# Kernel tuning notes

Measured on AMD Instinct MI355X. Metric: run time of the kernel, lower is better.

Reference implementation:

```python
import jax, jax.numpy as jnp
import numpy as np

N = 8192
N_DIM = 7
N_WIDTH = 64


def setup_inputs() -> dict:
    key = jax.random.key(0)
    ks = jax.random.split(key, 12)
    scale = 0.05
    u = lambda k, shape: scale * (2.0 * jax.random.uniform(k, shape) - 1.0)
    # Linear params stored as (in, out) so forward uses x @ W + b (same math as torch Linear).
    lin = lambda k, fan_in, fan_out: (
        jax.random.uniform(jax.random.fold_in(k, 0), (fan_in, fan_out),
                           minval=-1.0, maxval=1.0) / np.sqrt(fan_in),
        jax.random.uniform(jax.random.fold_in(k, 1), (fan_out,),
                           minval=-1.0, maxval=1.0) / np.sqrt(fan_in),
    )
    W1, b1 = lin(ks[1], N_DIM, N_WIDTH)
    W2, b2 = lin(ks[2], N_WIDTH, N_WIDTH)
    Wl, bl = lin(ks[3], N_WIDTH, 1)
    return {
        "x": jax.random.normal(ks[0], (N, N_DIM), dtype=jnp.float32),
        "alpha": jax.random.uniform(ks[4], (1,)),          # Edges.alpha = 1 * rand(1)
        "W1": W1, "b1": b1, "wt1": u(ks[5], (N_WIDTH, N_WIDTH)), "bs1": u(ks[6], (1,)),
        "W2": W2, "b2": b2, "wt2": u(ks[7], (N_WIDTH, N_WIDTH)), "bs2": u(ks[8], (1,)),
        "Wl": Wl, "bl": bl,
    }


def _edges(x, alpha):
    eta, phi = x[:, 1], x[:, 2]
    deta = eta[:, None] - eta[None, :]                      # (n, n)
    dphi = jnp.abs(phi[:, None] - phi[None, :])
    dphi = jnp.where(dphi > jnp.pi, 2.0 * jnp.pi - dphi, dphi)
    dRdR = deta * deta + dphi * dphi
    A = jnp.exp(-alpha[0] * dRdR)
    return jax.nn.softmax(A, axis=1) + jnp.eye(x.shape[0], dtype=x.dtype)


def _gcn_layer(X, A, W, b, wt, bs):
    X = jax.nn.relu(X @ W + b)                              # embed + relu
    X = (A @ X) @ wt + bs[0]                                # aggregate + mix + scalar bias
    return jax.nn.relu(X)


def reference(x, alpha, W1, b1, wt1, bs1, W2, b2, wt2, bs2, Wl, bl):
    A = _edges(x, alpha)
    V = jax.nn.relu(_gcn_layer(x, A, W1, b1, wt1, bs1))
    V = jax.nn.relu(_gcn_layer(V, A, W2, b2, wt2, bs2))
    s = V.sum(axis=0)                                       # (n_width,)
    return jax.nn.sigmoid(s @ Wl + bl)                      # (1,)
```

## Files before the change

kernel.cpp:

```cpp
#include <hip/hip_runtime.h>
#include <math.h>

#define NN 8192
#define L2E 1.44269504088896340736f
#define TWO_PI 6.28318530717958647693f

typedef _Float16 h8 __attribute__((ext_vector_type(8)));
typedef float f32x4 __attribute__((ext_vector_type(4)));
#define MFMA16(A, B, C) __builtin_amdgcn_mfma_f32_16x16x32_f16(A, B, C, 0, 0, 0)

#define GLD_LDS16(gsrc, ldst)                                          \
  __builtin_amdgcn_global_load_lds(                                    \
      (const __attribute__((address_space(1))) unsigned int*)(gsrc),   \
      (__attribute__((address_space(3))) unsigned int*)(ldst), 16, 0, 0)

union V8 { float4 v[2]; float f[8]; };
union AF { h8 v; decltype(__builtin_amdgcn_cvt_pkrtz(0.f, 0.f)) p[4]; };

__global__ __launch_bounds__(256) void prep_kernel(
    const float* __restrict__ x, const float* __restrict__ alpha,
    const float* __restrict__ W1, const float* __restrict__ b1,
    float* __restrict__ eta_s, float* __restrict__ phi_s,
    float* __restrict__ H1, _Float16* __restrict__ HT1,
    float* __restrict__ svec)
{
  __shared__ float sW[448];
  __shared__ float sb[64];
  __shared__ float T[32][65];
  const int t = threadIdx.x;
  if (blockIdx.x == 0 && t < 64) svec[t] = 0.f;
  for (int k = t; k < 448; k += 256) sW[k] = W1[k];
  if (t < 64) sb[t] = b1[t];
  const float s = sqrtf(alpha[0] * L2E);
  const int i0 = blockIdx.x * 32;
  const int r = t >> 3, q = t & 7;
  const int i = i0 + r;
  float xv[7];
#pragma unroll
  for (int k = 0; k < 7; k++) xv[k] = x[i * 7 + k];
  if (q == 0) { eta_s[i] = xv[1] * s; phi_s[i] = xv[2] * s; }
  __syncthreads();
#pragma unroll
  for (int c = 0; c < 8; c++) {
    const int n = q * 8 + c;
    float hv = sb[n];
#pragma unroll
    for (int k = 0; k < 7; k++) hv = fmaf(xv[k], sW[k * 64 + n], hv);
    T[r][n] = fmaxf(hv, 0.f);
  }
  __syncthreads();
  for (int e = t; e < 2048; e += 256) H1[i0 * 64 + e] = T[e >> 6][e & 63];
  const int n = t >> 2, sg = (t & 3) * 8;
  h8 v;
#pragma unroll
  for (int ss = 0; ss < 8; ss++) v[ss] = (_Float16)T[sg + ss][n];
  *(h8*)(HT1 + (size_t)n * NN + i0 + sg) = v;
}

template <int PASS>
__global__ __launch_bounds__(512, 4) void fused_pass(
    const float* __restrict__ eta_s, const float* __restrict__ phi_s,
    const _Float16* __restrict__ HTin, const float* __restrict__ Hres,
    const float* __restrict__ WA, const float* __restrict__ bsA,
    const float* __restrict__ WB, const float* __restrict__ bB,
    const float* __restrict__ alpha, float* __restrict__ lsum,
    float* __restrict__ Hout, _Float16* __restrict__ HTout,
    float* __restrict__ svec, const float* __restrict__ Wl,
    const float* __restrict__ bl, float* __restrict__ out,
    unsigned* __restrict__ bar)
{
  __shared__ __align__(16) char smem[65536];
  __shared__ unsigned last_ticket;
  _Float16* stage = (_Float16*)smem;
  const int tid = threadIdx.x;
  const int w = tid >> 6, lane = tid & 63, m = lane & 15, g = lane >> 4;
  const int i0 = blockIdx.x << 4;
  const float Cs = TWO_PI * sqrtf(alpha[0] * L2E);
  const float et0 = eta_s[i0 + m], ph0 = phi_s[i0 + m];

  const int rr = tid >> 5, gq = tid & 31;
  const _Float16* sb4[4];
#pragma unroll
  for (int k = 0; k < 4; ++k) {
    const int rowk = k * 16 + rr;
    sb4[k] = HTin + (size_t)rowk * NN + ((gq ^ (rowk & 31)) << 3);
  }
  int fo[4];
#pragma unroll
  for (int c = 0; c < 4; ++c) {
    const int row = c * 16 + m;
    fo[c] = row * 256 + ((((w << 2) | g) ^ (row & 31)) << 3);
  }

  f32x4 a0 = {0,0,0,0}, a1 = {0,0,0,0}, a2 = {0,0,0,0}, a3 = {0,0,0,0};
  float lacc = 0.f;

  const float* ep = eta_s + (w << 5) + (g << 3);
  const float* pp = phi_s + (w << 5) + (g << 3);
  V8 E, P, En, Pn;
  E.v[0] = *(const float4*)ep;  E.v[1] = *(const float4*)(ep + 4);
  P.v[0] = *(const float4*)pp;  P.v[1] = *(const float4*)(pp + 4);
  En = E; Pn = P;

#pragma unroll
  for (int k = 0; k < 4; ++k)
    GLD_LDS16(sb4[k], stage + ((k * 512 + tid) << 3));
  __syncthreads();

  for (int s = 0; s < 32; ++s) {
    _Float16* cur = stage + ((s & 1) << 14);
    if (s < 31) {
      _Float16* nxt = stage + (((s + 1) & 1) << 14);
      const int joff = (s + 1) * 256;
#pragma unroll
      for (int k = 0; k < 4; ++k)
        GLD_LDS16(sb4[k] + joff, nxt + ((k * 512 + tid) << 3));
      ep += 256; pp += 256;
      En.v[0] = *(const float4*)ep;  En.v[1] = *(const float4*)(ep + 4);
      Pn.v[0] = *(const float4*)pp;  Pn.v[1] = *(const float4*)(pp + 4);
    }
    const h8 b0 = *(const h8*)(cur + fo[0]);
    const h8 b1 = *(const h8*)(cur + fo[1]);
    const h8 b2 = *(const h8*)(cur + fo[2]);
    const h8 b3 = *(const h8*)(cur + fo[3]);

    AF af;
#pragma unroll
    for (int tt = 0; tt < 8; tt += 2) {
      float Pv[2];
#pragma unroll
      for (int u = 0; u < 2; ++u) {
        const float dp = ph0 - P.f[tt + u];
        const float ad = fabsf(dp);
        const float wr = fminf(ad, Cs - ad);
        const float de = et0 - E.f[tt + u];
        const float r2 = fmaf(de, de, wr * wr);
        const float a  = __builtin_amdgcn_exp2f(-r2);
        const float pv = __builtin_amdgcn_exp2f(fmaf(a, L2E, -L2E));
        if constexpr (PASS == 1) lacc += pv;
        Pv[u] = pv;
      }
      af.p[tt >> 1] = __builtin_amdgcn_cvt_pkrtz(Pv[0], Pv[1]);
    }
    a0 = MFMA16(af.v, b0, a0); a1 = MFMA16(af.v, b1, a1);
    a2 = MFMA16(af.v, b2, a2); a3 = MFMA16(af.v, b3, a3);
    E = En; P = Pn;
    __syncthreads();
  }

  float* RED  = (float*)smem;
  float* LRED = (float*)(smem + 34816);
  float* LROW = (float*)(smem + 36864);
  float* UBUF = (float*)(smem + 37120);
  float* ZBUF = (float*)(smem + 41728);

#pragma unroll
  for (int r = 0; r < 4; ++r) {
    const int rowi = (w * 16 + g * 4 + r) * 68;
    RED[rowi + m]      = a0[r];
    RED[rowi + 16 + m] = a1[r];
    RED[rowi + 32 + m] = a2[r];
    RED[rowi + 48 + m] = a3[r];
  }
  if constexpr (PASS == 1) LRED[((w << 2) | g) * 16 + m] = lacc;
  __syncthreads();

  const int r  = tid >> 5;
  const int c2 = (tid & 31) << 1;
  float y0 = 0.f, y1 = 0.f;
#pragma unroll
  for (int q = 0; q < 8; ++q) {
    y0 += RED[(q * 16 + r) * 68 + c2];
    y1 += RED[(q * 16 + r) * 68 + c2 + 1];
  }
  const float2 hres = *(const float2*)(Hres + (size_t)(i0 + r) * 64 + c2);
  if (tid < 16) {
    float lv;
    if constexpr (PASS == 1) {
      lv = 0.f;
#pragma unroll
      for (int q = 0; q < 32; ++q) lv += LRED[q * 16 + tid];
      lsum[i0 + tid] = lv;
    } else {
      lv = lsum[i0 + tid];
    }
    LROW[tid] = lv;
  }
  __syncthreads();

  const float rl = 1.0f / LROW[r];
  UBUF[r * 68 + c2]     = fmaf(y0, rl, hres.x);
  UBUF[r * 68 + c2 + 1] = fmaf(y1, rl, hres.y);
  __syncthreads();

  float z0 = bsA[0], z1 = z0;
  for (int k = 0; k < 64; ++k) {
    const float uk = UBUF[r * 68 + k];
    const float2 wv = *(const float2*)(WA + k * 64 + c2);
    z0 = fmaf(uk, wv.x, z0);
    z1 = fmaf(uk, wv.y, z1);
  }
  z0 = fmaxf(z0, 0.f); z1 = fmaxf(z1, 0.f);
  ZBUF[r * 68 + c2]     = z0;
  ZBUF[r * 68 + c2 + 1] = z1;
  __syncthreads();

  if constexpr (PASS == 1) {
    float h0 = bB[c2], h1 = bB[c2 + 1];
    for (int k = 0; k < 64; ++k) {
      const float zk = ZBUF[r * 68 + k];
      const float2 wv = *(const float2*)(WB + k * 64 + c2);
      h0 = fmaf(zk, wv.x, h0);
      h1 = fmaf(zk, wv.y, h1);
    }
    h0 = fmaxf(h0, 0.f); h1 = fmaxf(h1, 0.f);
    float2 hw; hw.x = h0; hw.y = h1;
    *(float2*)(Hout + (size_t)(i0 + r) * 64 + c2) = hw;
    UBUF[r * 68 + c2]     = h0;
    UBUF[r * 68 + c2 + 1] = h1;
    __syncthreads();
    const int n = tid >> 3, ri = (tid & 7) << 1;
    union { _Float16 hh[2]; unsigned u; } pk;
    pk.hh[0] = (_Float16)UBUF[ri * 68 + n];
    pk.hh[1] = (_Float16)UBUF[(ri + 1) * 68 + n];
    *(unsigned*)(HTout + (size_t)n * NN + i0 + ri) = pk.u;
  } else {
    if (tid < 64) {
      float cs = 0.f;
#pragma unroll
      for (int rw = 0; rw < 16; ++rw) cs += ZBUF[rw * 68 + tid];
      atomicAdd(svec + tid, cs);
    }
    __syncthreads();
    if (tid == 0)
      last_ticket = __hip_atomic_fetch_add(bar, 1u, __ATOMIC_RELAXED,
                                           __HIP_MEMORY_SCOPE_AGENT);
    __syncthreads();
    if (last_ticket == gridDim.x - 1) {
      if (tid == 0) __builtin_amdgcn_fence(__ATOMIC_ACQUIRE, "agent");
      __syncthreads();
      if (tid < 64) {
        float v = svec[tid] * Wl[tid];
#pragma unroll
        for (int off = 32; off > 0; off >>= 1) v += __shfl_down(v, off);
        if (tid == 0) {
          const float logit = v + bl[0];
          out[0] = 1.0f / (1.0f + __builtin_amdgcn_exp2f(-logit * L2E));
        }
      }
    }
  }
}

extern "C" void kernel_launch(void* const* d_in, const int* in_sizes, int n_in,
                              void* d_out, int out_size, void* d_ws,
                              size_t ws_size, hipStream_t stream)
{
  const float* x     = (const float*)d_in[0];
  const float* alpha = (const float*)d_in[1];
  const float* W1    = (const float*)d_in[2];
  const float* b1    = (const float*)d_in[3];
  const float* wt1   = (const float*)d_in[4];
  const float* bs1   = (const float*)d_in[5];
  const float* W2    = (const float*)d_in[6];
  const float* b2    = (const float*)d_in[7];
  const float* wt2   = (const float*)d_in[8];
  const float* bs2   = (const float*)d_in[9];
  const float* Wl    = (const float*)d_in[10];
  const float* bl    = (const float*)d_in[11];
  float* out = (float*)d_out;

  char* ws = (char*)d_ws;
  size_t off = 0;
  auto alloc = [&](size_t bytes) {
    void* p = ws + off;
    off = (off + bytes + 255) & ~(size_t)255;
    return p;
  };
  float* eta_s   = (float*)alloc(NN * 4 + 256);
  float* phi_s   = (float*)alloc(NN * 4 + 256);
  float* H1      = (float*)alloc((size_t)NN * 64 * 4);
  float* H2      = (float*)alloc((size_t)NN * 64 * 4);
  _Float16* HT1  = (_Float16*)alloc((size_t)NN * 64 * 2 + 512);
  _Float16* HT2  = (_Float16*)alloc((size_t)NN * 64 * 2 + 512);
  float* lsum    = (float*)alloc(NN * 4);
  float* svec    = (float*)alloc(64 * 4);
  unsigned* bar  = (unsigned*)alloc(256);

  hipMemsetAsync(bar, 0, 256, stream);
  prep_kernel<<<256, 256, 0, stream>>>(x, alpha, W1, b1, eta_s, phi_s, H1,
                                       HT1, svec);
  fused_pass<1><<<512, 512, 0, stream>>>(eta_s, phi_s, HT1, H1, wt1, bs1, W2,
                                         b2, alpha, lsum, H2, HT2, nullptr,
                                         nullptr, nullptr, nullptr, nullptr);
  fused_pass<2><<<512, 512, 0, stream>>>(eta_s, phi_s, HT2, H2, wt2, bs2,
                                         nullptr, nullptr, alpha, lsum,
                                         nullptr, nullptr, svec, Wl, bl, out,
                                         bar);
}
```

Baseline: 189.9 us.

## Load B operands directly to registers, drop LDS staging and per-step barriers

The main loop no longer stages the transposed feature matrix through double-buffered LDS with global_load_lds and a __syncthreads each step. Each wave now owns a contiguous 1024-column chunk of j and loads its MFMA B operands and eta/phi values straight into registers with one-step-ahead prefetch in a fully unrolled loop. This removes barriers and LDS traffic and lowers the LDS footprint, but it changes the j partitioning and adds register pressure and less coalesced strided global loads. The bar reset also moves from a separate memset into prep_kernel, saving one enqueue.

Measured after the change: 249.3 us. +31.3%, slower.

```diff
diff --git a/kernel.cpp b/kernel.cpp
--- a/kernel.cpp
+++ b/kernel.cpp
@@ -8,11 +8,6 @@
 typedef _Float16 h8 __attribute__((ext_vector_type(8)));
 typedef float f32x4 __attribute__((ext_vector_type(4)));
 #define MFMA16(A, B, C) __builtin_amdgcn_mfma_f32_16x16x32_f16(A, B, C, 0, 0, 0)
-
-#define GLD_LDS16(gsrc, ldst)                                          \
-  __builtin_amdgcn_global_load_lds(                                    \
-      (const __attribute__((address_space(1))) unsigned int*)(gsrc),   \
-      (__attribute__((address_space(3))) unsigned int*)(ldst), 16, 0, 0)
 
 union V8 { float4 v[2]; float f[8]; };
 union AF { h8 v; decltype(__builtin_amdgcn_cvt_pkrtz(0.f, 0.f)) p[4]; };
@@ -22,13 +17,16 @@
     const float* __restrict__ W1, const float* __restrict__ b1,
     float* __restrict__ eta_s, float* __restrict__ phi_s,
     float* __restrict__ H1, _Float16* __restrict__ HT1,
-    float* __restrict__ svec)
+    float* __restrict__ svec, unsigned* __restrict__ bar)
 {
   __shared__ float sW[448];
   __shared__ float sb[64];
   __shared__ float T[32][65];
   const int t = threadIdx.x;
-  if (blockIdx.x == 0 && t < 64) svec[t] = 0.f;
+  if (blockIdx.x == 0) {
+    if (t < 64) svec[t] = 0.f;
+    if (t == 64) bar[0] = 0u;
+  }
   for (int k = t; k < 448; k += 256) sW[k] = W1[k];
   if (t < 64) sb[t] = b1[t];
   const float s = sqrtf(alpha[0] * L2E);
@@ -69,71 +67,51 @@
     const float* __restrict__ bl, float* __restrict__ out,
     unsigned* __restrict__ bar)
 {
-  __shared__ __align__(16) char smem[65536];
+  __shared__ __align__(16) char smem[46080];
   __shared__ unsigned last_ticket;
-  _Float16* stage = (_Float16*)smem;
   const int tid = threadIdx.x;
   const int w = tid >> 6, lane = tid & 63, m = lane & 15, g = lane >> 4;
   const int i0 = blockIdx.x << 4;
   const float Cs = TWO_PI * sqrtf(alpha[0] * L2E);
   const float et0 = eta_s[i0 + m], ph0 = phi_s[i0 + m];
 
-  const int rr = tid >> 5, gq = tid & 31;
-  const _Float16* sb4[4];
-#pragma unroll
-  for (int k = 0; k < 4; ++k) {
-    const int rowk = k * 16 + rr;
-    sb4[k] = HTin + (size_t)rowk * NN + ((gq ^ (rowk & 31)) << 3);
-  }
-  int fo[4];
-#pragma unroll
-  for (int c = 0; c < 4; ++c) {
-    const int row = c * 16 + m;
-    fo[c] = row * 256 + ((((w << 2) | g) ^ (row & 31)) << 3);
-  }
+  const int jw = (w << 10) + (g << 3);
+  const _Float16* b0p = HTin + (size_t)(m)      * NN + jw;
+  const _Float16* b1p = HTin + (size_t)(16 + m) * NN + jw;
+  const _Float16* b2p = HTin + (size_t)(32 + m) * NN + jw;
+  const _Float16* b3p = HTin + (size_t)(48 + m) * NN + jw;
+  const float* ep = eta_s + jw;
+  const float* pp = phi_s + jw;
 
   f32x4 a0 = {0,0,0,0}, a1 = {0,0,0,0}, a2 = {0,0,0,0}, a3 = {0,0,0,0};
   float lacc = 0.f;
 
-  const float* ep = eta_s + (w << 5) + (g << 3);
-  const float* pp = phi_s + (w << 5) + (g << 3);
-  V8 E, P, En, Pn;
+  h8 b0 = *(const h8*)b0p, b1 = *(const h8*)b1p;
+  h8 b2 = *(const h8*)b2p, b3 = *(const h8*)b3p;
+  V8 E, P;
   E.v[0] = *(const float4*)ep;  E.v[1] = *(const float4*)(ep + 4);
   P.v[0] = *(const float4*)pp;  P.v[1] = *(const float4*)(pp + 4);
-  En = E; Pn = P;
-
-#pragma unroll
-  for (int k = 0; k < 4; ++k)
-    GLD_LDS16(sb4[k], stage + ((k * 512 + tid) << 3));
-  __syncthreads();
-
-  for (int s = 0; s < 32; ++s) {
-    _Float16* cur = stage + ((s & 1) << 14);
-    if (s < 31) {
-      _Float16* nxt = stage + (((s + 1) & 1) << 14);
-      const int joff = (s + 1) * 256;
-#pragma unroll
-      for (int k = 0; k < 4; ++k)
-        GLD_LDS16(sb4[k] + joff, nxt + ((k * 512 + tid) << 3));
-      ep += 256; pp += 256;
-      En.v[0] = *(const float4*)ep;  En.v[1] = *(const float4*)(ep + 4);
-      Pn.v[0] = *(const float4*)pp;  Pn.v[1] = *(const float4*)(pp + 4);
-    }
-    const h8 b0 = *(const h8*)(cur + fo[0]);
-    const h8 b1 = *(const h8*)(cur + fo[1]);
-    const h8 b2 = *(const h8*)(cur + fo[2]);
-    const h8 b3 = *(const h8*)(cur + fo[3]);
-
+
+#pragma unroll
+  for (int it = 0; it < 32; ++it) {
+    const h8 cb0 = b0, cb1 = b1, cb2 = b2, cb3 = b3;
+    const V8 CE = E, CP = P;
+    if (it < 31) {
+      const int o = (it + 1) * 32;
+      b0 = *(const h8*)(b0p + o); b1 = *(const h8*)(b1p + o);
+      b2 = *(const h8*)(b2p + o); b3 = *(const h8*)(b3p + o);
+      E.v[0] = *(const float4*)(ep + o); E.v[1] = *(const float4*)(ep + o + 4);
+      P.v[0] = *(const float4*)(pp + o); P.v[1] = *(const float4*)(pp + o + 4);
+    }
     AF af;
 #pragma unroll
     for (int tt = 0; tt < 8; tt += 2) {
       float Pv[2];
 #pragma unroll
       for (int u = 0; u < 2; ++u) {
-        const float dp = ph0 - P.f[tt + u];
-        const float ad = fabsf(dp);
-        const float wr = fminf(ad, Cs - ad);
-        const float de = et0 - E.f[tt + u];
+        const float dp = ph0 - CP.f[tt + u];
+        const float wr = fminf(fabsf(dp), Cs - fabsf(dp));
+        const float de = et0 - CE.f[tt + u];
         const float r2 = fmaf(de, de, wr * wr);
         const float a  = __builtin_amdgcn_exp2f(-r2);
         const float pv = __builtin_amdgcn_exp2f(fmaf(a, L2E, -L2E));
@@ -142,10 +120,8 @@
       }
       af.p[tt >> 1] = __builtin_amdgcn_cvt_pkrtz(Pv[0], Pv[1]);
     }
-    a0 = MFMA16(af.v, b0, a0); a1 = MFMA16(af.v, b1, a1);
-    a2 = MFMA16(af.v, b2, a2); a3 = MFMA16(af.v, b3, a3);
-    E = En; P = Pn;
-    __syncthreads();
+    a0 = MFMA16(af.v, cb0, a0); a1 = MFMA16(af.v, cb1, a1);
+    a2 = MFMA16(af.v, cb2, a2); a3 = MFMA16(af.v, cb3, a3);
   }
 
   float* RED  = (float*)smem;
@@ -277,8 +253,8 @@
     off = (off + bytes + 255) & ~(size_t)255;
     return p;
   };
-  float* eta_s   = (float*)alloc(NN * 4 + 256);
-  float* phi_s   = (float*)alloc(NN * 4 + 256);
+  float* eta_s   = (float*)alloc(NN * 4 + 512);
+  float* phi_s   = (float*)alloc(NN * 4 + 512);
   float* H1      = (float*)alloc((size_t)NN * 64 * 4);
   float* H2      = (float*)alloc((size_t)NN * 64 * 4);
   _Float16* HT1  = (_Float16*)alloc((size_t)NN * 64 * 2 + 512);
@@ -287,9 +263,8 @@
   float* svec    = (float*)alloc(64 * 4);
   unsigned* bar  = (unsigned*)alloc(256);
 
-  hipMemsetAsync(bar, 0, 256, stream);
   prep_kernel<<<256, 256, 0, stream>>>(x, alpha, W1, b1, eta_s, phi_s, H1,
-                                       HT1, svec);
+                                       HT1, svec, bar);
   fused_pass<1><<<512, 512, 0, stream>>>(eta_s, phi_s, HT1, H1, wt1, bs1, W2,
                                          b2, alpha, lsum, H2, HT2, nullptr,
                                          nullptr, nullptr, nullptr, nullptr);
```
